# Optimization experiments

Hardware: AMD Instinct MI355X
Metric: run time of the kernel (lower is better)

## Reference

```python
import jax, jax.numpy as jnp
import numpy as np

ALPHA = 16.0
K = 32
NUM_INSTANCES = 8  # samples per class in the batch (required by the original reshape logic)


def setup_inputs() -> dict:
    key = jax.random.key(0)
    n, d = 4096, 128
    inputs = jax.random.normal(key, (n, d), dtype=jnp.float32)
    # identity-sampler style labels: each class appears exactly NUM_INSTANCES times,
    # as assumed by the original pos_dist.resize(...) logic
    targets = (jnp.arange(n) // NUM_INSTANCES).astype(jnp.int64)
    return {"inputs": inputs, "targets": targets}


def reference(inputs, targets):
    n = inputs.shape[0]
    # L2-normalize rows (normalized=True)
    x = inputs / jnp.linalg.norm(inputs, axis=1, keepdims=True)
    # squared euclidean distance matrix: ||xi||^2 + ||xj||^2 - 2 xi.xj
    sq = jnp.sum(x * x, axis=1)  # [n]
    dist = sq[:, None] + sq[None, :] - 2.0 * (x @ x.T)  # [n, n]

    eye = jnp.eye(n, dtype=bool)
    same = targets[:, None] == targets[None, :]
    pos_mask = same & ~eye          # positives, excluding self
    neg_mask = ~same                # negatives

    inf = jnp.float32(jnp.inf)
    # threshold = K-th smallest (0-indexed) among the n-1 off-diagonal dists per row
    row_sorted = jnp.sort(jnp.where(eye, inf, dist), axis=1)
    thr = row_sorted[:, K]  # [n]

    base = jnp.mean(dist, axis=1, keepdims=True)  # mean over full row (incl. diagonal 0)
    below = dist < thr[:, None]
    pos_sel = pos_mask & below
    neg_sel = neg_mask & below

    expo = jnp.exp(ALPHA * (base - dist))  # [n, n]
    pos_logit = jnp.sum(jnp.where(pos_sel, expo, 0.0), axis=1)
    neg_logit = jnp.sum(jnp.where(neg_sel, expo, 0.0), axis=1)

    # fallback when no positive is below the threshold: use the closest positive
    min_pos = jnp.min(jnp.where(pos_mask, dist, inf), axis=1)
    fallback = jnp.exp(ALPHA * (base[:, 0] - min_pos))
    has_pos = jnp.any(pos_sel, axis=1)
    pos_logit = jnp.where(has_pos, pos_logit, fallback)

    loss_i = -jnp.log(pos_logit / (pos_logit + neg_logit))  # [n]
    loss = jnp.mean(loss_i)
    accuracy = jnp.mean((loss_i < 0.6).astype(jnp.float32))
    pos_d = jnp.sum(jnp.where(pos_mask, dist, 0.0)) / jnp.sum(pos_mask)
    neg_d = jnp.sum(jnp.where(neg_mask, dist, 0.0)) / jnp.sum(neg_mask)
    return loss, accuracy, pos_d, neg_d
```

## Files before the change

### kernel.cpp

```cpp
#include <hip/hip_runtime.h>
#include <math.h>

#define N 4096
#define D 128
#define KSEL 32
#define ALPHA_C 16.0f

typedef short bf16x8 __attribute__((ext_vector_type(8)));
typedef float f32x4  __attribute__((ext_vector_type(4)));

__device__ inline float waveSumF(float v){
  #pragma unroll
  for (int o = 32; o; o >>= 1) v += __shfl_xor(v, o);
  return v;
}
__device__ inline int waveSumI(int v){
  #pragma unroll
  for (int o = 32; o; o >>= 1) v += __shfl_xor(v, o);
  return v;
}
__device__ inline float waveMinF(float v){
  #pragma unroll
  for (int o = 32; o; o >>= 1) v = fminf(v, __shfl_xor(v, o));
  return v;
}
__device__ inline unsigned fkey(float f){
  unsigned u = __float_as_uint(f);
  return u ^ ((u >> 31) ? 0xFFFFFFFFu : 0x80000000u);
}
__device__ inline float fkey_inv(unsigned u){
  unsigned bits = (u & 0x80000000u) ? (u ^ 0x80000000u) : ~u;
  return __uint_as_float(bits);
}
__device__ inline unsigned short f2bf(float x){
  unsigned u = __float_as_uint(x);
  return (unsigned short)((u + 0x7FFFu + ((u >> 16) & 1u)) >> 16);
}
__device__ inline float bf2f(unsigned short h){
  return __uint_as_float(((unsigned)h) << 16);
}

__global__ __launch_bounds__(256) void knorm(const float* __restrict__ in,
                                             unsigned short* __restrict__ xh,
                                             unsigned short* __restrict__ xl,
                                             float* __restrict__ sq,
                                             double* __restrict__ accum,
                                             unsigned* __restrict__ ctr){
  if (blockIdx.x == 0 && threadIdx.x < 5){
    if (threadIdx.x < 4) accum[threadIdx.x] = 0.0;
    else *ctr = 0u;
  }
  const int row  = blockIdx.x * 4 + (threadIdx.x >> 6);
  const int lane = threadIdx.x & 63;
  const float* p = in + (size_t)row * D;
  float e0 = p[lane], e1 = p[lane + 64];
  float s = waveSumF(e0*e0 + e1*e1);
  float inv = 1.0f / sqrtf(s);
  float x0 = e0 * inv, x1 = e1 * inv;
  float s2 = waveSumF(x0*x0 + x1*x1);
  unsigned short h0 = f2bf(x0);  unsigned short l0 = f2bf(x0 - bf2f(h0));
  unsigned short h1 = f2bf(x1);  unsigned short l1 = f2bf(x1 - bf2f(h1));
  xh[(size_t)row * D + lane]      = h0;
  xh[(size_t)row * D + lane + 64] = h1;
  xl[(size_t)row * D + lane]      = l0;
  xl[(size_t)row * D + lane + 64] = l1;
  if (lane == 0) sq[row] = s2;
}

__global__ __launch_bounds__(512, 2) void kdot(const unsigned short* __restrict__ xh,
                                               const unsigned short* __restrict__ xl,
                                               const float* __restrict__ sq,
                                               float* __restrict__ dist){
  const int lane = threadIdx.x & 63;
  const int w    = threadIdx.x >> 6;
  const int wr   = w >> 2, wc = w & 3;
  const int i0   = blockIdx.y * 128;
  const int j0   = blockIdx.x * 128;

  const int rA = i0 + 64*wr + (lane & 15);
  const int cB = j0 + 32*wc + (lane & 15);
  const int kb = (lane >> 4) * 8;

  f32x4 acc[4][2];
  #pragma unroll
  for (int tr = 0; tr < 4; ++tr)
    #pragma unroll
    for (int tc = 0; tc < 2; ++tc) acc[tr][tc] = (f32x4){0.f,0.f,0.f,0.f};

  #pragma unroll
  for (int ks = 0; ks < 4; ++ks){
    const int k = 32*ks + kb;
    bf16x8 ah[4], al[4], bh[2], bl[2];
    #pragma unroll
    for (int tr = 0; tr < 4; ++tr){
      ah[tr] = *(const bf16x8*)(xh + (size_t)(rA + 16*tr) * D + k);
      al[tr] = *(const bf16x8*)(xl + (size_t)(rA + 16*tr) * D + k);
    }
    #pragma unroll
    for (int tc = 0; tc < 2; ++tc){
      bh[tc] = *(const bf16x8*)(xh + (size_t)(cB + 16*tc) * D + k);
      bl[tc] = *(const bf16x8*)(xl + (size_t)(cB + 16*tc) * D + k);
    }
    #pragma unroll
    for (int tr = 0; tr < 4; ++tr)
      #pragma unroll
      for (int tc = 0; tc < 2; ++tc){
        acc[tr][tc] = __builtin_amdgcn_mfma_f32_16x16x32_bf16(ah[tr], bh[tc], acc[tr][tc], 0, 0, 0);
        acc[tr][tc] = __builtin_amdgcn_mfma_f32_16x16x32_bf16(ah[tr], bl[tc], acc[tr][tc], 0, 0, 0);
        acc[tr][tc] = __builtin_amdgcn_mfma_f32_16x16x32_bf16(al[tr], bh[tc], acc[tr][tc], 0, 0, 0);
      }
  }

  const int icol = i0 + 64*wr + 4*(lane >> 4);
  const int jrow = j0 + 32*wc + (lane & 15);
  #pragma unroll
  for (int tr = 0; tr < 4; ++tr){
    const int ib = icol + 16*tr;
    const float4 sqi4 = *(const float4*)(sq + ib);
    #pragma unroll
    for (int tc = 0; tc < 2; ++tc){
      const int j = jrow + 16*tc;
      const float sqj = sq[j];
      float4 v;
      v.x = sqi4.x + sqj - 2.0f * acc[tr][tc][0];
      v.y = sqi4.y + sqj - 2.0f * acc[tr][tc][1];
      v.z = sqi4.z + sqj - 2.0f * acc[tr][tc][2];
      v.w = sqi4.w + sqj - 2.0f * acc[tr][tc][3];
      *(float4*)(dist + (size_t)j * N + ib) = v;
    }
  }
}

__global__ __launch_bounds__(512, 2) void ksel(const float* __restrict__ dist,
                                               const int* __restrict__ tgt,
                                               double* __restrict__ accum,
                                               unsigned* __restrict__ ctr,
                                               float* __restrict__ out){
  __shared__ float scrP[8], scrN[8], lsSh[8], acSh[8];

  const int tid  = threadIdx.x;
  const int lane = tid & 63;
  const int w    = tid >> 6;
  const int r    = blockIdx.x * 8 + w;

  const int tw = tgt[r];
  const float4* drow = (const float4*)(dist + (size_t)r * N);
  const int4*   tg4  = (const int4*)tgt;

  float d[64];
  float pb = 0.f, posd = 0.f, negd = 0.f, pm = INFINITY;
  #pragma unroll
  for (int u = 0; u < 16; ++u){
    float4 v = drow[64*u + lane];
    int4  tg = tg4 [64*u + lane];
    const int jb = 4*(64*u + lane);
    #pragma unroll
    for (int q = 0; q < 4; ++q){
      float dj = (q==0)?v.x:(q==1)?v.y:(q==2)?v.z:v.w;
      int   tj = (q==0)?tg.x:(q==1)?tg.y:(q==2)?tg.z:tg.w;
      const bool diag = (jb + q == r);
      pb += dj;
      const bool same = (tj == tw);
      if (same && !diag){ posd += dj; pm = fminf(pm, dj); }
      if (!same) negd += dj;
      d[4*u + q] = diag ? INFINITY : dj;
    }
  }
  const float base   = waveSumF(pb) * (1.0f / (float)N);
  const float minpos = waveMinF(pm);
  { float v = waveSumF(posd); if (lane == 0) scrP[w] = v; }
  { float v = waveSumF(negd); if (lane == 0) scrN[w] = v; }

  float thr;
  {
    float dmin = INFINITY;
    #pragma unroll
    for (int s = 0; s < 64; ++s) dmin = fminf(dmin, d[s]);
    dmin = waveMinF(dmin);

    unsigned lo = fkey(dmin);
    unsigned hi = fkey(4.5f);
    while (hi - lo > 1u){
      float loV = fkey_inv(lo), hiV = fkey_inv(hi);
      unsigned mid = fkey(0.5f * (loV + hiV));
      mid = (mid <= lo) ? lo + 1u : ((mid >= hi) ? hi - 1u : mid);
      float pv = fkey_inv(mid);
      int cc = 0;
      #pragma unroll
      for (int s = 0; s < 64; ++s) cc += (d[s] < pv) ? 1 : 0;
      cc = waveSumI(cc);
      if (cc < KSEL + 1) lo = mid;
      else hi = mid;
    }
    thr = fkey_inv(lo);
  }

  {
    float pls = 0.f, nls = 0.f; int pcnt = 0;
    #pragma unroll
    for (int u = 0; u < 16; ++u){
      int4 tg = tg4[64*u + lane];
      #pragma unroll
      for (int q = 0; q < 4; ++q){
        float dvq = d[4*u + q];
        int   tj  = (q==0)?tg.x:(q==1)?tg.y:(q==2)?tg.z:tg.w;
        if (dvq < thr){
          float e = expf(ALPHA_C * (base - dvq));
          if (tj == tw){ pls += e; pcnt++; } else nls += e;
        }
      }
    }
    pls = waveSumF(pls); nls = waveSumF(nls); pcnt = waveSumI(pcnt);
    if (lane == 0){
      float plogit = (pcnt > 0) ? pls : expf(ALPHA_C * (base - minpos));
      float li = -logf(plogit / (plogit + nls));
      lsSh[w] = li;
      acSh[w] = (li < 0.6f) ? 1.f : 0.f;
    }
  }
  __syncthreads();
  if (tid == 0){
    float ls = 0.f, ac = 0.f; double sp = 0.0, sn = 0.0;
    #pragma unroll
    for (int q = 0; q < 8; ++q){
      ls += lsSh[q]; ac += acSh[q];
      sp += (double)scrP[q]; sn += (double)scrN[q];
    }
    atomicAdd(&accum[0], (double)ls);
    atomicAdd(&accum[1], (double)ac);
    atomicAdd(&accum[2], sp);
    atomicAdd(&accum[3], sn);
    __threadfence();
    unsigned done = atomicAdd(ctr, 1u);
    if (done == gridDim.x - 1){
      double a0 = atomicAdd(&accum[0], 0.0);
      double a1 = atomicAdd(&accum[1], 0.0);
      double a2 = atomicAdd(&accum[2], 0.0);
      double a3 = atomicAdd(&accum[3], 0.0);
      out[0] = (float)(a0 / (double)N);
      out[1] = (float)(a1 / (double)N);
      out[2] = (float)(a2 / ((double)N * 7.0));
      out[3] = (float)(a3 / ((double)N * (double)(N - 8)));
    }
  }
}

extern "C" void kernel_launch(void* const* d_in, const int* in_sizes, int n_in,
                              void* d_out, int out_size, void* d_ws, size_t ws_size,
                              hipStream_t stream){
  (void)in_sizes; (void)n_in; (void)out_size; (void)ws_size;
  const float* in  = (const float*)d_in[0];
  const int*   tgt = (const int*)d_in[1];
  float* out = (float*)d_out;

  char* ws = (char*)d_ws;
  unsigned short* xh = (unsigned short*)(ws);
  unsigned short* xl = (unsigned short*)(ws + 1048576);
  float*    sq    = (float*)(ws + 2097152);
  double*   accum = (double*)(ws + 2113536);
  unsigned* ctr   = (unsigned*)(ws + 2113568);
  float*    dist  = (float*)(ws + 2113792);

  knorm<<<N/4, 256, 0, stream>>>(in, xh, xl, sq, accum, ctr);
  dim3 g(N/128, N/128);
  kdot <<<g, 512, 0, stream>>>(xh, xl, sq, dist);
  ksel <<<N/8, 512, 0, stream>>>(dist, tgt, accum, ctr, out);
}
```

Before: 203.0 us.

## Quantize distance matrix to 16-bit fixed point and simplify threshold search

The distance kernel now writes distances as 16-bit fixed-point values, staged through shared memory so stores are row-major and coalesced, with the diagonal forced to max. The selection kernel reads these halves plus 16-bit labels, keeps a per-lane same-class bitmask, and does a 16-step integer bisection on the quantized grid for the K-th threshold. This halves the traffic of the large intermediate matrix. In exchange, distances and the threshold are rounded to 1/16384, which perturbs the exponentials slightly.

After: 164.8 us. 1.23x faster.

```diff
diff --git a/kernel.cpp b/kernel.cpp
--- a/kernel.cpp
+++ b/kernel.cpp
@@ -5,6 +5,8 @@
 #define D 128
 #define KSEL 32
 #define ALPHA_C 16.0f
+#define QS  16384.0f
+#define QSI (1.0f/16384.0f)
 
 typedef short bf16x8 __attribute__((ext_vector_type(8)));
 typedef float f32x4  __attribute__((ext_vector_type(4)));
@@ -23,14 +25,6 @@
   #pragma unroll
   for (int o = 32; o; o >>= 1) v = fminf(v, __shfl_xor(v, o));
   return v;
-}
-__device__ inline unsigned fkey(float f){
-  unsigned u = __float_as_uint(f);
-  return u ^ ((u >> 31) ? 0xFFFFFFFFu : 0x80000000u);
-}
-__device__ inline float fkey_inv(unsigned u){
-  unsigned bits = (u & 0x80000000u) ? (u ^ 0x80000000u) : ~u;
-  return __uint_as_float(bits);
 }
 __device__ inline unsigned short f2bf(float x){
   unsigned u = __float_as_uint(x);
@@ -41,9 +35,11 @@
 }
 
 __global__ __launch_bounds__(256) void knorm(const float* __restrict__ in,
+                                             const int* __restrict__ tgt,
                                              unsigned short* __restrict__ xh,
                                              unsigned short* __restrict__ xl,
                                              float* __restrict__ sq,
+                                             unsigned short* __restrict__ t16,
                                              double* __restrict__ accum,
                                              unsigned* __restrict__ ctr){
   if (blockIdx.x == 0 && threadIdx.x < 5){
@@ -64,13 +60,14 @@
   xh[(size_t)row * D + lane + 64] = h1;
   xl[(size_t)row * D + lane]      = l0;
   xl[(size_t)row * D + lane + 64] = l1;
-  if (lane == 0) sq[row] = s2;
+  if (lane == 0){ sq[row] = s2; t16[row] = (unsigned short)tgt[row]; }
 }
 
 __global__ __launch_bounds__(512, 2) void kdot(const unsigned short* __restrict__ xh,
                                                const unsigned short* __restrict__ xl,
                                                const float* __restrict__ sq,
-                                               float* __restrict__ dist){
+                                               unsigned short* __restrict__ dq){
+  __shared__ unsigned short til[128][136];
   const int lane = threadIdx.x & 63;
   const int w    = threadIdx.x >> 6;
   const int wr   = w >> 2, wc = w & 3;
@@ -111,27 +108,40 @@
       }
   }
 
-  const int icol = i0 + 64*wr + 4*(lane >> 4);
-  const int jrow = j0 + 32*wc + (lane & 15);
+  const int il_base = 64*wr + 4*(lane >> 4);
+  const int jl_base = 32*wc + (lane & 15);
   #pragma unroll
   for (int tr = 0; tr < 4; ++tr){
-    const int ib = icol + 16*tr;
-    const float4 sqi4 = *(const float4*)(sq + ib);
+    const int il4 = il_base + 16*tr;
+    const float4 sqi4 = *(const float4*)(sq + i0 + il4);
     #pragma unroll
     for (int tc = 0; tc < 2; ++tc){
-      const int j = jrow + 16*tc;
-      const float sqj = sq[j];
-      float4 v;
-      v.x = sqi4.x + sqj - 2.0f * acc[tr][tc][0];
-      v.y = sqi4.y + sqj - 2.0f * acc[tr][tc][1];
-      v.z = sqi4.z + sqj - 2.0f * acc[tr][tc][2];
-      v.w = sqi4.w + sqj - 2.0f * acc[tr][tc][3];
-      *(float4*)(dist + (size_t)j * N + ib) = v;
-    }
-  }
-}
-
-__global__ __launch_bounds__(512, 2) void ksel(const float* __restrict__ dist,
+      const int jl = jl_base + 16*tc;
+      const float sqj = sq[j0 + jl];
+      #pragma unroll
+      for (int reg = 0; reg < 4; ++reg){
+        const float sqi = (reg==0)?sqi4.x:(reg==1)?sqi4.y:(reg==2)?sqi4.z:sqi4.w;
+        float v = sqi + sqj - 2.0f * acc[tr][tc][reg];
+        int q = (int)(v * QS + 0.5f);
+        q = (q < 0) ? 0 : ((q > 65535) ? 65535 : q);
+        if (i0 + il4 + reg == j0 + jl) q = 65535;
+        til[il4 + reg][jl] = (unsigned short)q;
+      }
+    }
+  }
+  __syncthreads();
+
+  #pragma unroll
+  for (int it = 0; it < 4; ++it){
+    const int row = (threadIdx.x >> 4) + 32 * it;
+    const int col = (threadIdx.x & 15) * 8;
+    uint4 v = *(const uint4*)&til[row][col];
+    *(uint4*)(dq + (size_t)(i0 + row) * N + j0 + col) = v;
+  }
+}
+
+__global__ __launch_bounds__(512, 2) void ksel(const unsigned short* __restrict__ dq,
+                                               const unsigned short* __restrict__ t16,
                                                const int* __restrict__ tgt,
                                                double* __restrict__ accum,
                                                unsigned* __restrict__ ctr,
@@ -144,26 +154,33 @@
   const int r    = blockIdx.x * 8 + w;
 
   const int tw = tgt[r];
-  const float4* drow = (const float4*)(dist + (size_t)r * N);
-  const int4*   tg4  = (const int4*)tgt;
+  const uint4* qrow = (const uint4*)(dq + (size_t)r * N);
+  const uint4* trow = (const uint4*)t16;
 
   float d[64];
+  unsigned long long sameMask = 0ull;
   float pb = 0.f, posd = 0.f, negd = 0.f, pm = INFINITY;
-  #pragma unroll
-  for (int u = 0; u < 16; ++u){
-    float4 v = drow[64*u + lane];
-    int4  tg = tg4 [64*u + lane];
-    const int jb = 4*(64*u + lane);
-    #pragma unroll
-    for (int q = 0; q < 4; ++q){
-      float dj = (q==0)?v.x:(q==1)?v.y:(q==2)?v.z:v.w;
-      int   tj = (q==0)?tg.x:(q==1)?tg.y:(q==2)?tg.z:tg.w;
-      const bool diag = (jb + q == r);
-      pb += dj;
+
+  #pragma unroll
+  for (int u = 0; u < 8; ++u){
+    const uint4 q4 = qrow[lane + 64*u];
+    const uint4 t4 = trow[lane + 64*u];
+    const int jb = (lane + 64*u) * 8;
+    #pragma unroll
+    for (int k = 0; k < 8; ++k){
+      const unsigned qdw = (k<2)?q4.x:(k<4)?q4.y:(k<6)?q4.z:q4.w;
+      const unsigned tdw = (k<2)?t4.x:(k<4)?t4.y:(k<6)?t4.z:t4.w;
+      const unsigned q  = (k & 1) ? (qdw >> 16) : (qdw & 0xFFFFu);
+      const int      tj = (int)((k & 1) ? (tdw >> 16) : (tdw & 0xFFFFu));
+      const float dj = (float)q * QSI;
+      const bool diag = (jb + k == r);
       const bool same = (tj == tw);
+      if (!diag) pb += dj;
       if (same && !diag){ posd += dj; pm = fminf(pm, dj); }
       if (!same) negd += dj;
-      d[4*u + q] = diag ? INFINITY : dj;
+      const int s = 8*u + k;
+      d[s] = diag ? INFINITY : dj;
+      if (same) sameMask |= 1ull << s;
     }
   }
   const float base   = waveSumF(pb) * (1.0f / (float)N);
@@ -171,49 +188,34 @@
   { float v = waveSumF(posd); if (lane == 0) scrP[w] = v; }
   { float v = waveSumF(negd); if (lane == 0) scrN[w] = v; }
 
-  float thr;
+  float thrV;
   {
-    float dmin = INFINITY;
-    #pragma unroll
-    for (int s = 0; s < 64; ++s) dmin = fminf(dmin, d[s]);
-    dmin = waveMinF(dmin);
-
-    unsigned lo = fkey(dmin);
-    unsigned hi = fkey(4.5f);
+    unsigned lo = 0u, hi = 65536u;
     while (hi - lo > 1u){
-      float loV = fkey_inv(lo), hiV = fkey_inv(hi);
-      unsigned mid = fkey(0.5f * (loV + hiV));
-      mid = (mid <= lo) ? lo + 1u : ((mid >= hi) ? hi - 1u : mid);
-      float pv = fkey_inv(mid);
+      const unsigned mid = (lo + hi) >> 1;
+      const float pv = (float)mid * QSI;
       int cc = 0;
       #pragma unroll
       for (int s = 0; s < 64; ++s) cc += (d[s] < pv) ? 1 : 0;
       cc = waveSumI(cc);
-      if (cc < KSEL + 1) lo = mid;
-      else hi = mid;
-    }
-    thr = fkey_inv(lo);
+      if (cc < KSEL + 1) lo = mid; else hi = mid;
+    }
+    thrV = (float)lo * QSI;
   }
 
   {
     float pls = 0.f, nls = 0.f; int pcnt = 0;
     #pragma unroll
-    for (int u = 0; u < 16; ++u){
-      int4 tg = tg4[64*u + lane];
-      #pragma unroll
-      for (int q = 0; q < 4; ++q){
-        float dvq = d[4*u + q];
-        int   tj  = (q==0)?tg.x:(q==1)?tg.y:(q==2)?tg.z:tg.w;
-        if (dvq < thr){
-          float e = expf(ALPHA_C * (base - dvq));
-          if (tj == tw){ pls += e; pcnt++; } else nls += e;
-        }
+    for (int s = 0; s < 64; ++s){
+      if (d[s] < thrV){
+        const float e = expf(ALPHA_C * (base - d[s]));
+        if ((sameMask >> s) & 1ull){ pls += e; pcnt++; } else nls += e;
       }
     }
     pls = waveSumF(pls); nls = waveSumF(nls); pcnt = waveSumI(pcnt);
     if (lane == 0){
-      float plogit = (pcnt > 0) ? pls : expf(ALPHA_C * (base - minpos));
-      float li = -logf(plogit / (plogit + nls));
+      const float plogit = (pcnt > 0) ? pls : expf(ALPHA_C * (base - minpos));
+      const float li = -logf(plogit / (plogit + nls));
       lsSh[w] = li;
       acSh[w] = (li < 0.6f) ? 1.f : 0.f;
     }
@@ -254,15 +256,16 @@
   float* out = (float*)d_out;
 
   char* ws = (char*)d_ws;
-  unsigned short* xh = (unsigned short*)(ws);
-  unsigned short* xl = (unsigned short*)(ws + 1048576);
-  float*    sq    = (float*)(ws + 2097152);
-  double*   accum = (double*)(ws + 2113536);
-  unsigned* ctr   = (unsigned*)(ws + 2113568);
-  float*    dist  = (float*)(ws + 2113792);
-
-  knorm<<<N/4, 256, 0, stream>>>(in, xh, xl, sq, accum, ctr);
+  unsigned short* xh  = (unsigned short*)(ws);
+  unsigned short* xl  = (unsigned short*)(ws + 1048576);
+  float*          sq  = (float*)(ws + 2097152);
+  unsigned short* t16 = (unsigned short*)(ws + 2113536);
+  double*       accum = (double*)(ws + 2121728);
+  unsigned*       ctr = (unsigned*)(ws + 2121760);
+  unsigned short* dq  = (unsigned short*)(ws + 2129920);
+
+  knorm<<<N/4, 256, 0, stream>>>(in, tgt, xh, xl, sq, t16, accum, ctr);
   dim3 g(N/128, N/128);
-  kdot <<<g, 512, 0, stream>>>(xh, xl, sq, dist);
-  ksel <<<N/8, 512, 0, stream>>>(dist, tgt, accum, ctr, out);
-}
+  kdot <<<g, 512, 0, stream>>>(xh, xl, sq, dq);
+  ksel <<<N/8, 512, 0, stream>>>(dq, t16, tgt, accum, ctr, out);
+}
```
